# Optimization experiments

Measured on AMD Instinct MI355X. Metric: run time of the kernel, lower is better.

## Reference

```python
import jax, jax.numpy as jnp
import numpy as np

D_MODEL = 1024
N_HEADS = 16
HEAD_DIM = D_MODEL // N_HEADS
LAMBDA_MAX = 10.0
ALPHA = 5.0
EPS = 1e-8


def setup_inputs() -> dict:
    key = jax.random.key(0)
    ks = jax.random.split(key, 12)
    B, S, D = 4, 2048, D_MODEL
    x = jax.random.normal(ks[0], (B, S, D), dtype=jnp.float32)
    prior_mask = jax.random.normal(ks[1], (S, S), dtype=jnp.float32)
    # small perturbation so u ~ 0.05 -> lambda ~ 7.8 > 1 and clipping path is active
    delta_x = 0.05 * jax.random.normal(ks[2], (B, S, D), dtype=jnp.float32)
    scale = 1.0 / np.sqrt(D)
    wq = jax.random.normal(ks[3], (D, D), dtype=jnp.float32) * scale
    bq = jnp.zeros((D,), dtype=jnp.float32)
    wk = jax.random.normal(ks[4], (D, D), dtype=jnp.float32) * scale
    bk = jnp.zeros((D,), dtype=jnp.float32)
    wv = jax.random.normal(ks[5], (D, D), dtype=jnp.float32) * scale
    bv = jnp.zeros((D,), dtype=jnp.float32)
    wo = jax.random.normal(ks[6], (D, D), dtype=jnp.float32) * scale
    bo = jnp.zeros((D,), dtype=jnp.float32)
    return {"x": x, "prior_mask": prior_mask, "delta_x": delta_x,
            "wq": wq, "bq": bq, "wk": wk, "bk": bk,
            "wv": wv, "bv": bv, "wo": wo, "bo": bo}


def reference(x, prior_mask, delta_x, wq, bq, wk, bk, wv, bv, wo, bo):
    B, S, D = x.shape
    H, hd = N_HEADS, HEAD_DIM
    # projections (nn.Linear: x @ W^T + b), reshaped to [B, H, S, hd]
    Q = (x @ wq.T + bq).reshape(B, S, H, hd)
    K = (x @ wk.T + bk).reshape(B, S, H, hd)
    V = (x @ wv.T + bv).reshape(B, S, H, hd)
    A = jnp.einsum('bqhd,bkhd->bhqk', Q, K) / np.sqrt(hd).astype(np.float32)

    # ResidualSurprise
    norm_x = jnp.linalg.norm(x, axis=-1, keepdims=True)            # [B,S,1]
    norm_dx = jnp.linalg.norm(delta_x, axis=-1, keepdims=True)     # [B,S,1]
    u = norm_dx / (norm_x + EPS)                                   # [B,S,1]
    aggregated_u = u.mean(axis=1)                                  # [B,1]
    lam = LAMBDA_MAX * jnp.exp(-ALPHA * aggregated_u)              # [B,1]
    lam4 = lam.reshape(B, 1, 1, 1)

    Bias = prior_mask[None, None, :, :] * lam4                     # [B,1,S,S]
    L = A + Bias                                                    # [B,H,S,S]
    threshold = Bias.mean(axis=-1, keepdims=True)                  # [B,1,S,1]
    clip = (lam4 > 1.0) & (L < threshold)
    L = jnp.where(clip, -jnp.inf, L)

    attn = jax.nn.softmax(L, axis=-1)
    out = jnp.einsum('bhqk,bkhd->bqhd', attn, V).reshape(B, S, D)
    out = out @ wo.T + bo
    return out
```

## Files before the change

### kernel.cpp

```cpp
#include <hip/hip_runtime.h>
#include <hip/hip_bf16.h>

typedef unsigned short u16;
typedef unsigned int u32;
typedef unsigned long long u64;
typedef __attribute__((ext_vector_type(4))) float f32x4;
typedef __attribute__((ext_vector_type(8))) short s16x8;

#define D_MODEL 1024
#define NHEADS 16
#define HD 64
#define SEQ 2048
#define BATCH 4
#define ROWS (BATCH*SEQ)

#define MFMA16 __builtin_amdgcn_mfma_f32_16x16x32_bf16

__device__ inline u16 f2bf(float f) {
  u32 u = __builtin_bit_cast(u32, f);
  u32 r = (u + 0x7fffu + ((u >> 16) & 1u)) >> 16;
  return (u16)r;
}

__device__ inline u32 cvt_pk_bf16(float lo, float hi) {
  u32 r;
  asm volatile("v_cvt_pk_bf16_f32 %0, %1, %2" : "=v"(r) : "v"(lo), "v"(hi));
  return r;
}

__device__ inline void gload_lds16(const void* g, void* l) {
  __builtin_amdgcn_global_load_lds((const __attribute__((address_space(1))) void*)g,
                                   (__attribute__((address_space(3))) void*)l,
                                   16, 0, 0);
}


__global__ __launch_bounds__(256) void cast_f32_bf16(const float* __restrict__ src,
                                                     u16* __restrict__ dst, int n4) {
  int i = blockIdx.x * 256 + threadIdx.x;
  if (i >= n4) return;
  float4 v = ((const float4*)src)[i];
  union { u16 s[4]; u64 ll; } o;
  o.s[0] = f2bf(v.x); o.s[1] = f2bf(v.y); o.s[2] = f2bf(v.z); o.s[3] = f2bf(v.w);
  ((u64*)dst)[i] = o.ll;
}

__global__ __launch_bounds__(256) void row_u(const float* __restrict__ x,
                                             const float* __restrict__ dx,
                                             float* __restrict__ usum) {
  int row = blockIdx.x;
  int tid = threadIdx.x;
  const float4* xr = (const float4*)(x + (size_t)row * D_MODEL);
  const float4* dr = (const float4*)(dx + (size_t)row * D_MODEL);
  float4 a = xr[tid], d = dr[tid];
  float sx = a.x*a.x + a.y*a.y + a.z*a.z + a.w*a.w;
  float sd = d.x*d.x + d.y*d.y + d.z*d.z + d.w*d.w;
  #pragma unroll
  for (int m = 1; m < 64; m <<= 1) { sx += __shfl_xor(sx, m); sd += __shfl_xor(sd, m); }
  __shared__ float rx[4], rd[4];
  int wave = tid >> 6;
  if ((tid & 63) == 0) { rx[wave] = sx; rd[wave] = sd; }
  __syncthreads();
  if (tid == 0) {
    float SX = rx[0]+rx[1]+rx[2]+rx[3];
    float SD = rd[0]+rd[1]+rd[2]+rd[3];
    float u = sqrtf(SD) / (sqrtf(SX) + 1e-8f);
    atomicAdd(&usum[row >> 11], u);
  }
}

__global__ __launch_bounds__(256) void pm_rowmean_k(const float* __restrict__ pm,
                                                    float* __restrict__ pmrow) {
  int row = blockIdx.x, tid = threadIdx.x;
  const float4* pr = (const float4*)(pm + (size_t)row * SEQ);
  float4 a = pr[tid*2], b = pr[tid*2+1];
  float s = a.x+a.y+a.z+a.w + b.x+b.y+b.z+b.w;
  #pragma unroll
  for (int m = 1; m < 64; m <<= 1) s += __shfl_xor(s, m);
  __shared__ float rs[4];
  int wave = tid >> 6;
  if ((tid & 63) == 0) rs[wave] = s;
  __syncthreads();
  if (tid == 0) pmrow[row] = (rs[0]+rs[1]+rs[2]+rs[3]) * (1.0f / SEQ);
}

__global__ void lam_k(const float* __restrict__ usum, float* __restrict__ lam) {
  int t = threadIdx.x;
  if (t < BATCH) lam[t] = 10.0f * expf(-5.0f * usum[t] * (1.0f / SEQ));
}


__device__ inline void store_o(float* C, size_t i, float v) { C[i] = v; }
__device__ inline void store_o(u16* C, size_t i, float v)   { C[i] = f2bf(v); }

template<typename OutT, bool ROWB>
__global__ __launch_bounds__(256) void gemm_bt(const u16* __restrict__ A,
                                               const u16* __restrict__ Bw,
                                               const float* __restrict__ bias,
                                               OutT* __restrict__ C,
                                               int M, int N, int K) {
  __shared__ __align__(16) u16 As[128*32];
  __shared__ __align__(16) u16 Bs[128*32];
  const int tid = threadIdx.x;
  const int wave = tid >> 6, lane = tid & 63, g = lane >> 4, l15 = lane & 15;
  const int id0 = blockIdx.y * gridDim.x + blockIdx.x;
  const int cpx = (gridDim.x * gridDim.y) >> 3;
  const int id = (id0 & 7) * cpx + (id0 >> 3);
  const int bx = id % gridDim.x, by = id / gridDim.x;
  const int row0 = by * 128, col0 = bx * 128;
  const int wr = (wave >> 1) * 64, wc = (wave & 1) * 64;
  f32x4 acc[4][4] = {};
  const int chunk0 = wave * 2048;
  for (int k0 = 0; k0 < K; k0 += 32) {
    #pragma unroll
    for (int c = 0; c < 2; ++c) {
      int chunk = chunk0 + c * 1024;
      int li = chunk + lane * 16;
      int r = li >> 6;
      int cb = (li & 63) >> 1;
      const u16* ga = A  + (size_t)(row0 + r) * K + k0 + cb;
      gload_lds16(ga, (char*)As + chunk);
      const u16* gb = Bw + (size_t)(col0 + r) * K + k0 + cb;
      gload_lds16(gb, (char*)Bs + chunk);
    }
    __syncthreads();
    s16x8 af[4], bf[4];
    #pragma unroll
    for (int mi = 0; mi < 4; ++mi) af[mi] = *(const s16x8*)&As[(wr + mi*16 + l15)*32 + g*8];
    #pragma unroll
    for (int ni = 0; ni < 4; ++ni) bf[ni] = *(const s16x8*)&Bs[(wc + ni*16 + l15)*32 + g*8];
    __builtin_amdgcn_s_setprio(1);
    #pragma unroll
    for (int mi = 0; mi < 4; ++mi)
      #pragma unroll
      for (int ni = 0; ni < 4; ++ni)
        acc[mi][ni] = MFMA16(af[mi], bf[ni], acc[mi][ni], 0, 0, 0);
    __builtin_amdgcn_s_setprio(0);
    __syncthreads();
  }
  #pragma unroll
  for (int mi = 0; mi < 4; ++mi) {
    int rbase = row0 + wr + mi*16 + g*4;
    #pragma unroll
    for (int ni = 0; ni < 4; ++ni) {
      int cc = col0 + wc + ni*16 + l15;
      float cbias = ROWB ? 0.0f : bias[cc];
      #pragma unroll
      for (int r = 0; r < 4; ++r) {
        float v = acc[mi][ni][r] + (ROWB ? bias[rbase + r] : cbias);
        store_o(C, (size_t)(rbase + r) * N + cc, v);
      }
    }
  }
}


__global__ __launch_bounds__(256) void attn_k(const u16* __restrict__ Qb,
                                              const u16* __restrict__ Kb,
                                              const u16* __restrict__ Vtb,
                                              const float* __restrict__ pm,
                                              const float* __restrict__ pmrow,
                                              const float* __restrict__ lamp,
                                              u16* __restrict__ Ob) {
  __shared__ __align__(16) u16 Ks[2][64*64];
  __shared__ __align__(16) u16 Vs[2][64*64];
  __shared__ __align__(16) u16 Ps[4][32*72];
  const int id0 = blockIdx.y * gridDim.x + blockIdx.x;
  const int id = (id0 & 7) * 128 + (id0 >> 3);
  const int bh = id & 63, qt = id >> 6;
  const int b = bh >> 4, h = bh & 15;
  const int tid = threadIdx.x, wave = tid >> 6, lane = tid & 63;
  const int g = lane >> 4, l15 = lane & 15;
  const float lam = lamp[b];
  const bool clip_en = lam > 1.0f;
  const int q0 = qt * 128 + wave * 32;

  s16x8 qf[2][2];
  #pragma unroll
  for (int mi = 0; mi < 2; ++mi)
    #pragma unroll
    for (int kk = 0; kk < 2; ++kk)
      qf[mi][kk] = *(const s16x8*)&Qb[(size_t)(b*SEQ + q0 + mi*16 + l15)*D_MODEL + h*HD + kk*32 + g*8];

  float thr[2], mrow[2], lrow[2];
  #pragma unroll
  for (int mi = 0; mi < 2; ++mi) {
    thr[mi] = clip_en ? lam * pmrow[q0 + mi*16 + l15] : -INFINITY;
    mrow[mi] = -INFINITY;
    lrow[mi] = 0.0f;
  }
  f32x4 oacc[2][4] = {};

  #define STAGE(buf, kt) do {                                                   \
    _Pragma("unroll")                                                           \
    for (int c = 0; c < 2; ++c) {                                               \
      int chunk = wave * 2048 + c * 1024;                                       \
      int li = chunk + lane * 16;                                               \
      int r_ = li >> 7;                                                         \
      int ccol = (li & 127) >> 4;                                               \
      int gcol = ((ccol ^ (r_ & 7)) * 8);                                       \
      const u16* gk = Kb  + (size_t)(b*SEQ + (kt) + r_)*D_MODEL + h*HD + gcol;  \
      gload_lds16(gk, (char*)Ks[buf] + chunk);                                  \
      const u16* gv = Vtb + (size_t)(h*HD + r_)*ROWS + b*SEQ + (kt) + gcol;     \
      gload_lds16(gv, (char*)Vs[buf] + chunk);                                  \
    } } while (0)

  STAGE(0, 0);
  __syncthreads();
  int cur = 0;

  for (int kt = 0; kt < SEQ; kt += 64) {
    if (kt + 64 < SEQ) STAGE(cur ^ 1, kt + 64);

    f32x4 s[2][4] = {};
    #pragma unroll
    for (int nj = 0; nj < 4; ++nj) {
      int row = nj*16 + l15;
      s16x8 kf0 = *(const s16x8*)((const char*)Ks[cur] + row*128 + (((0*4 + g) ^ (row & 7)) * 16));
      s16x8 kf1 = *(const s16x8*)((const char*)Ks[cur] + row*128 + (((1*4 + g) ^ (row & 7)) * 16));
      __builtin_amdgcn_s_setprio(1);
      #pragma unroll
      for (int mi = 0; mi < 2; ++mi) {
        s[mi][nj] = MFMA16(kf0, qf[mi][0], s[mi][nj], 0, 0, 0);
        s[mi][nj] = MFMA16(kf1, qf[mi][1], s[mi][nj], 0, 0, 0);
      }
      __builtin_amdgcn_s_setprio(0);
    }

    #pragma unroll
    for (int mi = 0; mi < 2; ++mi) {
      const int qrow = q0 + mi*16 + l15;
      const float* pmr = pm + (size_t)qrow * SEQ + kt;
      float Lv[4][4];
      float mx = -INFINITY;
      #pragma unroll
      for (int nj = 0; nj < 4; ++nj) {
        float4 pv = *(const float4*)(pmr + nj*16 + g*4);
        float pa[4] = {pv.x, pv.y, pv.z, pv.w};
        #pragma unroll
        for (int r = 0; r < 4; ++r) {
          float L = s[mi][nj][r] * 0.125f + lam * pa[r];
          L = (L < thr[mi]) ? -INFINITY : L;
          Lv[nj][r] = L;
          mx = fmaxf(mx, L);
        }
      }
      mx = fmaxf(mx, __shfl_xor(mx, 16));
      mx = fmaxf(mx, __shfl_xor(mx, 32));
      float mnew = fmaxf(mrow[mi], mx);
      float rs = 0.0f, scale;
      if (mnew == -INFINITY) {
        scale = 1.0f;
        #pragma unroll
        for (int nj = 0; nj < 4; ++nj)
          #pragma unroll
          for (int r = 0; r < 4; ++r) Lv[nj][r] = 0.0f;
      } else {
        scale = __expf(mrow[mi] - mnew);
        #pragma unroll
        for (int nj = 0; nj < 4; ++nj)
          #pragma unroll
          for (int r = 0; r < 4; ++r) {
            float p = __expf(Lv[nj][r] - mnew);
            Lv[nj][r] = p;
            rs += p;
          }
      }
      rs += __shfl_xor(rs, 16);
      rs += __shfl_xor(rs, 32);
      lrow[mi] = lrow[mi] * scale + rs;
      mrow[mi] = mnew;
      #pragma unroll
      for (int di = 0; di < 4; ++di)
        #pragma unroll
        for (int r = 0; r < 4; ++r) oacc[mi][di][r] *= scale;
      #pragma unroll
      for (int nj = 0; nj < 4; ++nj) {
        u32 d0 = cvt_pk_bf16(Lv[nj][0], Lv[nj][1]);
        u32 d1 = cvt_pk_bf16(Lv[nj][2], Lv[nj][3]);
        u64 w = (u64)d0 | ((u64)d1 << 32);
        *(u64*)&Ps[wave][(mi*16 + l15)*72 + nj*16 + g*4] = w;
      }
    }

    s16x8 pf[2][2];
    #pragma unroll
    for (int mi = 0; mi < 2; ++mi)
      #pragma unroll
      for (int kk = 0; kk < 2; ++kk)
        pf[mi][kk] = *(const s16x8*)&Ps[wave][(mi*16 + l15)*72 + kk*32 + g*8];
    s16x8 vf[4][2];
    #pragma unroll
    for (int di = 0; di < 4; ++di) {
      int row = di*16 + l15;
      #pragma unroll
      for (int kk = 0; kk < 2; ++kk)
        vf[di][kk] = *(const s16x8*)((const char*)Vs[cur] + row*128 + (((kk*4 + g) ^ (row & 7)) * 16));
    }
    __builtin_amdgcn_s_setprio(1);
    #pragma unroll
    for (int mi = 0; mi < 2; ++mi)
      #pragma unroll
      for (int di = 0; di < 4; ++di)
        #pragma unroll
        for (int kk = 0; kk < 2; ++kk)
          oacc[mi][di] = MFMA16(vf[di][kk], pf[mi][kk], oacc[mi][di], 0, 0, 0);
    __builtin_amdgcn_s_setprio(0);
    __syncthreads();
    cur ^= 1;
  }
  #undef STAGE

  #pragma unroll
  for (int mi = 0; mi < 2; ++mi) {
    float inv = 1.0f / lrow[mi];
    size_t base = (size_t)(b*SEQ + q0 + mi*16 + l15) * D_MODEL + h*HD;
    #pragma unroll
    for (int di = 0; di < 4; ++di) {
      u32 d0 = cvt_pk_bf16(oacc[mi][di][0] * inv, oacc[mi][di][1] * inv);
      u32 d1 = cvt_pk_bf16(oacc[mi][di][2] * inv, oacc[mi][di][3] * inv);
      u64 w = (u64)d0 | ((u64)d1 << 32);
      *(u64*)&Ob[base + di*16 + g*4] = w;
    }
  }
}


extern "C" void kernel_launch(void* const* d_in, const int* in_sizes, int n_in,
                              void* d_out, int out_size, void* d_ws, size_t ws_size,
                              hipStream_t stream) {
  const float* x  = (const float*)d_in[0];
  const float* pm = (const float*)d_in[1];
  const float* dx = (const float*)d_in[2];
  const float* wq = (const float*)d_in[3];
  const float* bq = (const float*)d_in[4];
  const float* wk = (const float*)d_in[5];
  const float* bk = (const float*)d_in[6];
  const float* wv = (const float*)d_in[7];
  const float* bv = (const float*)d_in[8];
  const float* wo = (const float*)d_in[9];
  const float* bo = (const float*)d_in[10];
  float* out = (float*)d_out;

  char* ws = (char*)d_ws;
  const size_t MB = 1024 * 1024;
  u16* xb   = (u16*)(ws + 0 * MB);
  u16* Qb   = (u16*)(ws + 16 * MB);
  u16* Kb   = (u16*)(ws + 32 * MB);
  u16* Vtb  = (u16*)(ws + 48 * MB);
  u16* Obuf = (u16*)(ws + 64 * MB);
  u16* wqb  = (u16*)(ws + 80 * MB);
  u16* wkb  = (u16*)(ws + 82 * MB);
  u16* wvb  = (u16*)(ws + 84 * MB);
  u16* wob  = (u16*)(ws + 86 * MB);
  float* pmrow = (float*)(ws + 88 * MB);
  float* usum  = (float*)(ws + 88 * MB + 16384);
  float* lam   = (float*)(ws + 88 * MB + 16384 + 64);

  hipMemsetAsync(usum, 0, 16, stream);
  cast_f32_bf16<<<8192, 256, 0, stream>>>(x,  xb,  ROWS * D_MODEL / 4);
  cast_f32_bf16<<<1024, 256, 0, stream>>>(wq, wqb, D_MODEL * D_MODEL / 4);
  cast_f32_bf16<<<1024, 256, 0, stream>>>(wk, wkb, D_MODEL * D_MODEL / 4);
  cast_f32_bf16<<<1024, 256, 0, stream>>>(wv, wvb, D_MODEL * D_MODEL / 4);
  cast_f32_bf16<<<1024, 256, 0, stream>>>(wo, wob, D_MODEL * D_MODEL / 4);
  row_u<<<ROWS, 256, 0, stream>>>(x, dx, usum);
  pm_rowmean_k<<<SEQ, 256, 0, stream>>>(pm, pmrow);
  lam_k<<<1, 64, 0, stream>>>(usum, lam);

  gemm_bt<u16, false><<<dim3(8, 64), 256, 0, stream>>>(xb, wqb, bq, Qb, ROWS, D_MODEL, D_MODEL);
  gemm_bt<u16, false><<<dim3(8, 64), 256, 0, stream>>>(xb, wkb, bk, Kb, ROWS, D_MODEL, D_MODEL);
  gemm_bt<u16, true ><<<dim3(64, 8), 256, 0, stream>>>(wvb, xb, bv, Vtb, D_MODEL, ROWS, D_MODEL);

  attn_k<<<dim3(64, 16), 256, 0, stream>>>(Qb, Kb, Vtb, pm, pmrow, lam, Obuf);

  gemm_bt<float, false><<<dim3(8, 64), 256, 0, stream>>>(Obuf, wob, bo, out, ROWS, D_MODEL, D_MODEL);
}
```

Baseline: 614.6 us.

## Fold softmax scale into Q projection, use exp2 with lazy rescale, double-buffer GEMM

The Q projection epilogue now multiplies by 0.125*log2(e), and lambda is prescaled by log2(e), so attention computes logits directly in the base-2 domain and calls the hardware exp2. The online-softmax rescale of the accumulator is skipped unless the wave-wide max grows by more than a threshold. Prior-mask loads are issued before the QK MFMAs so their latency can overlap the matrix work. The projection GEMMs gain a double-buffered LDS pipeline with one barrier per k-step. Together these cut ALU work in the softmax loop and memory stalls in the GEMMs, at the cost of more LDS and a slightly different rounding, since Q is scaled before the bf16 cast.

```diff
diff --git a/kernel.cpp b/kernel.cpp
--- a/kernel.cpp
+++ b/kernel.cpp
@@ -15,6 +15,8 @@
 #define ROWS (BATCH*SEQ)
 
 #define MFMA16 __builtin_amdgcn_mfma_f32_16x16x32_bf16
+#define LOG2E 1.4426950408889634f
+#define THR2 11.5416f
 
 __device__ inline u16 f2bf(float f) {
   u32 u = __builtin_bit_cast(u32, f);
@@ -98,9 +100,9 @@
                                                const u16* __restrict__ Bw,
                                                const float* __restrict__ bias,
                                                OutT* __restrict__ C,
-                                               int M, int N, int K) {
-  __shared__ __align__(16) u16 As[128*32];
-  __shared__ __align__(16) u16 Bs[128*32];
+                                               int M, int N, int K, float oscale) {
+  __shared__ __align__(16) u16 As[2][128*32];
+  __shared__ __align__(16) u16 Bs[2][128*32];
   const int tid = threadIdx.x;
   const int wave = tid >> 6, lane = tid & 63, g = lane >> 4, l15 = lane & 15;
   const int id0 = blockIdx.y * gridDim.x + blockIdx.x;
@@ -111,24 +113,28 @@
   const int wr = (wave >> 1) * 64, wc = (wave & 1) * 64;
   f32x4 acc[4][4] = {};
   const int chunk0 = wave * 2048;
+
+  #define GSTAGE(buf, k0) do {                                          \
+    _Pragma("unroll")                                                   \
+    for (int c = 0; c < 2; ++c) {                                       \
+      int chunk = chunk0 + c * 1024;                                    \
+      int li = chunk + lane * 16;                                       \
+      int r_ = li >> 6;                                                 \
+      int cb = (li & 63) >> 1;                                          \
+      gload_lds16(A  + (size_t)(row0 + r_) * K + (k0) + cb, (char*)As[buf] + chunk); \
+      gload_lds16(Bw + (size_t)(col0 + r_) * K + (k0) + cb, (char*)Bs[buf] + chunk); \
+    } } while (0)
+
+  GSTAGE(0, 0);
+  __syncthreads();
+  int cur = 0;
   for (int k0 = 0; k0 < K; k0 += 32) {
-    #pragma unroll
-    for (int c = 0; c < 2; ++c) {
-      int chunk = chunk0 + c * 1024;
-      int li = chunk + lane * 16;
-      int r = li >> 6;
-      int cb = (li & 63) >> 1;
-      const u16* ga = A  + (size_t)(row0 + r) * K + k0 + cb;
-      gload_lds16(ga, (char*)As + chunk);
-      const u16* gb = Bw + (size_t)(col0 + r) * K + k0 + cb;
-      gload_lds16(gb, (char*)Bs + chunk);
-    }
-    __syncthreads();
+    if (k0 + 32 < K) GSTAGE(cur ^ 1, k0 + 32);
     s16x8 af[4], bf[4];
     #pragma unroll
-    for (int mi = 0; mi < 4; ++mi) af[mi] = *(const s16x8*)&As[(wr + mi*16 + l15)*32 + g*8];
-    #pragma unroll
-    for (int ni = 0; ni < 4; ++ni) bf[ni] = *(const s16x8*)&Bs[(wc + ni*16 + l15)*32 + g*8];
+    for (int mi = 0; mi < 4; ++mi) af[mi] = *(const s16x8*)&As[cur][(wr + mi*16 + l15)*32 + g*8];
+    #pragma unroll
+    for (int ni = 0; ni < 4; ++ni) bf[ni] = *(const s16x8*)&Bs[cur][(wc + ni*16 + l15)*32 + g*8];
     __builtin_amdgcn_s_setprio(1);
     #pragma unroll
     for (int mi = 0; mi < 4; ++mi)
@@ -137,7 +143,10 @@
         acc[mi][ni] = MFMA16(af[mi], bf[ni], acc[mi][ni], 0, 0, 0);
     __builtin_amdgcn_s_setprio(0);
     __syncthreads();
-  }
+    cur ^= 1;
+  }
+  #undef GSTAGE
+
   #pragma unroll
   for (int mi = 0; mi < 4; ++mi) {
     int rbase = row0 + wr + mi*16 + g*4;
@@ -147,7 +156,7 @@
       float cbias = ROWB ? 0.0f : bias[cc];
       #pragma unroll
       for (int r = 0; r < 4; ++r) {
-        float v = acc[mi][ni][r] + (ROWB ? bias[rbase + r] : cbias);
+        float v = (acc[mi][ni][r] + (ROWB ? bias[rbase + r] : cbias)) * oscale;
         store_o(C, (size_t)(rbase + r) * N + cc, v);
       }
     }
@@ -172,6 +181,7 @@
   const int tid = threadIdx.x, wave = tid >> 6, lane = tid & 63;
   const int g = lane >> 4, l15 = lane & 15;
   const float lam = lamp[b];
+  const float lam2 = lam * LOG2E;
   const bool clip_en = lam > 1.0f;
   const int q0 = qt * 128 + wave * 32;
 
@@ -185,7 +195,7 @@
   float thr[2], mrow[2], lrow[2];
   #pragma unroll
   for (int mi = 0; mi < 2; ++mi) {
-    thr[mi] = clip_en ? lam * pmrow[q0 + mi*16 + l15] : -INFINITY;
+    thr[mi] = clip_en ? lam2 * pmrow[q0 + mi*16 + l15] : -INFINITY;
     mrow[mi] = -INFINITY;
     lrow[mi] = 0.0f;
   }
@@ -212,12 +222,21 @@
   for (int kt = 0; kt < SEQ; kt += 64) {
     if (kt + 64 < SEQ) STAGE(cur ^ 1, kt + 64);
 
+    float4 pv[2][4];
+    #pragma unroll
+    for (int mi = 0; mi < 2; ++mi) {
+      const float* pmr = pm + (size_t)(q0 + mi*16 + l15) * SEQ + kt;
+      #pragma unroll
+      for (int nj = 0; nj < 4; ++nj)
+        pv[mi][nj] = *(const float4*)(pmr + nj*16 + g*4);
+    }
+
     f32x4 s[2][4] = {};
     #pragma unroll
     for (int nj = 0; nj < 4; ++nj) {
       int row = nj*16 + l15;
-      s16x8 kf0 = *(const s16x8*)((const char*)Ks[cur] + row*128 + (((0*4 + g) ^ (row & 7)) * 16));
-      s16x8 kf1 = *(const s16x8*)((const char*)Ks[cur] + row*128 + (((1*4 + g) ^ (row & 7)) * 16));
+      s16x8 kf0 = *(const s16x8*)((const char*)Ks[cur] + row*128 + ((g ^ (row & 7)) * 16));
+      s16x8 kf1 = *(const s16x8*)((const char*)Ks[cur] + row*128 + (((4 + g) ^ (row & 7)) * 16));
       __builtin_amdgcn_s_setprio(1);
       #pragma unroll
       for (int mi = 0; mi < 2; ++mi) {
@@ -229,55 +248,47 @@
 
     #pragma unroll
     for (int mi = 0; mi < 2; ++mi) {
-      const int qrow = q0 + mi*16 + l15;
-      const float* pmr = pm + (size_t)qrow * SEQ + kt;
-      float Lv[4][4];
       float mx = -INFINITY;
       #pragma unroll
       for (int nj = 0; nj < 4; ++nj) {
-        float4 pv = *(const float4*)(pmr + nj*16 + g*4);
-        float pa[4] = {pv.x, pv.y, pv.z, pv.w};
+        float pa[4] = {pv[mi][nj].x, pv[mi][nj].y, pv[mi][nj].z, pv[mi][nj].w};
         #pragma unroll
         for (int r = 0; r < 4; ++r) {
-          float L = s[mi][nj][r] * 0.125f + lam * pa[r];
-          L = (L < thr[mi]) ? -INFINITY : L;
-          Lv[nj][r] = L;
+          float L = fmaf(lam2, pa[r], s[mi][nj][r]);
+          s[mi][nj][r] = L;
           mx = fmaxf(mx, L);
         }
       }
       mx = fmaxf(mx, __shfl_xor(mx, 16));
       mx = fmaxf(mx, __shfl_xor(mx, 32));
-      float mnew = fmaxf(mrow[mi], mx);
-      float rs = 0.0f, scale;
-      if (mnew == -INFINITY) {
-        scale = 1.0f;
+      if (__any(mx > mrow[mi] + THR2)) {
+        float mnew = fmaxf(mrow[mi], mx);
+        float scale = __builtin_amdgcn_exp2f(mrow[mi] - mnew);
+        lrow[mi] *= scale;
         #pragma unroll
-        for (int nj = 0; nj < 4; ++nj)
+        for (int di = 0; di < 4; ++di)
           #pragma unroll
-          for (int r = 0; r < 4; ++r) Lv[nj][r] = 0.0f;
-      } else {
-        scale = __expf(mrow[mi] - mnew);
+          for (int r = 0; r < 4; ++r) oacc[mi][di][r] *= scale;
+        mrow[mi] = mnew;
+      }
+      const float m = mrow[mi];
+      float rs = 0.0f;
+      #pragma unroll
+      for (int nj = 0; nj < 4; ++nj)
         #pragma unroll
-        for (int nj = 0; nj < 4; ++nj)
-          #pragma unroll
-          for (int r = 0; r < 4; ++r) {
-            float p = __expf(Lv[nj][r] - mnew);
-            Lv[nj][r] = p;
-            rs += p;
-          }
-      }
+        for (int r = 0; r < 4; ++r) {
+          float L = s[mi][nj][r];
+          float p = (L < thr[mi]) ? 0.0f : __builtin_amdgcn_exp2f(L - m);
+          s[mi][nj][r] = p;
+          rs += p;
+        }
       rs += __shfl_xor(rs, 16);
       rs += __shfl_xor(rs, 32);
-      lrow[mi] = lrow[mi] * scale + rs;
-      mrow[mi] = mnew;
-      #pragma unroll
-      for (int di = 0; di < 4; ++di)
-        #pragma unroll
-        for (int r = 0; r < 4; ++r) oacc[mi][di][r] *= scale;
+      lrow[mi] += rs;
       #pragma unroll
       for (int nj = 0; nj < 4; ++nj) {
-        u32 d0 = cvt_pk_bf16(Lv[nj][0], Lv[nj][1]);
-        u32 d1 = cvt_pk_bf16(Lv[nj][2], Lv[nj][3]);
+        u32 d0 = cvt_pk_bf16(s[mi][nj][0], s[mi][nj][1]);
+        u32 d1 = cvt_pk_bf16(s[mi][nj][2], s[mi][nj][3]);
         u64 w = (u64)d0 | ((u64)d1 << 32);
         *(u64*)&Ps[wave][(mi*16 + l15)*72 + nj*16 + g*4] = w;
       }
@@ -357,6 +368,8 @@
   float* usum  = (float*)(ws + 88 * MB + 16384);
   float* lam   = (float*)(ws + 88 * MB + 16384 + 64);
 
+  const float QSCALE = 0.125f * LOG2E;
+
   hipMemsetAsync(usum, 0, 16, stream);
   cast_f32_bf16<<<8192, 256, 0, stream>>>(x,  xb,  ROWS * D_MODEL / 4);
   cast_f32_bf16<<<1024, 256, 0, stream>>>(wq, wqb, D_MODEL * D_MODEL / 4);
@@ -367,11 +380,11 @@
   pm_rowmean_k<<<SEQ, 256, 0, stream>>>(pm, pmrow);
   lam_k<<<1, 64, 0, stream>>>(usum, lam);
 
-  gemm_bt<u16, false><<<dim3(8, 64), 256, 0, stream>>>(xb, wqb, bq, Qb, ROWS, D_MODEL, D_MODEL);
-  gemm_bt<u16, false><<<dim3(8, 64), 256, 0, stream>>>(xb, wkb, bk, Kb, ROWS, D_MODEL, D_MODEL);
-  gemm_bt<u16, true ><<<dim3(64, 8), 256, 0, stream>>>(wvb, xb, bv, Vtb, D_MODEL, ROWS, D_MODEL);
+  gemm_bt<u16, false><<<dim3(8, 64), 256, 0, stream>>>(xb, wqb, bq, Qb, ROWS, D_MODEL, D_MODEL, QSCALE);
+  gemm_bt<u16, false><<<dim3(8, 64), 256, 0, stream>>>(xb, wkb, bk, Kb, ROWS, D_MODEL, D_MODEL, 1.0f);
+  gemm_bt<u16, true ><<<dim3(64, 8), 256, 0, stream>>>(wvb, xb, bv, Vtb, D_MODEL, ROWS, D_MODEL, 1.0f);
 
   attn_k<<<dim3(64, 16), 256, 0, stream>>>(Qb, Kb, Vtb, pm, pmrow, lam, Obuf);
 
-  gemm_bt<float, false><<<dim3(8, 64), 256, 0, stream>>>(Obuf, wob, bo, out, ROWS, D_MODEL, D_MODEL);
-}
+  gemm_bt<float, false><<<dim3(8, 64), 256, 0, stream>>>(Obuf, wob, bo, out, ROWS, D_MODEL, D_MODEL, 1.0f);
+}
```

Result: faster. 545.6 us (-11.2%).
